# Performance work log

Hardware: AMD Instinct MI355X
Metric: run time of the kernel (lower is better)

The kernel has to match this reference:

```python
import jax, jax.numpy as jnp
import numpy as np

N_REACHES = 4096
N_STEPS = 96
DT = 3600.0  # routing timestep (s), default from MuskingumCungeRouter


def safe_pow(base, exp, eps=1e-6):
    # AD-safe power: exp(e * log(max(b, eps)))
    return jnp.exp(exp * jnp.log(jnp.maximum(base, eps)))


def setup_inputs() -> dict:
    key = jax.random.key(0)
    ks = jax.random.split(key, 10)
    n, T = N_REACHES, N_STEPS
    u = lambda k, lo, hi, shape: jax.random.uniform(k, shape, minval=lo, maxval=hi)
    lateral_inflows = u(ks[0], 0.0, 5.0, (T, n))          # m^3/s lateral inflow
    initial_Q = u(ks[1], 0.1, 10.0, (n,))
    lengths = u(ks[2], 500.0, 10000.0, (n,))              # reach length (m)
    slopes = u(ks[3], 1e-4, 0.05, (n,))                   # bed slope
    manning_n = u(ks[4], 0.02, 0.08, (n,))
    width_coef = u(ks[5], 2.0, 10.0, (n,))
    width_exp = u(ks[6], 0.4, 0.6, (n,))                  # ~0.5 typical
    depth_coef = u(ks[7], 0.2, 0.6, (n,))
    depth_exp = u(ks[8], 0.25, 0.35, (n,))                # ~0.3 typical
    # Strictly lower-triangular sparse adjacency: reach i receives from j < i
    # (valid topological order), ~4 upstream links per reach on average.
    upstream_mask = jnp.tril(jax.random.uniform(ks[9], (n, n)) < (4.0 / n), k=-1)
    is_outlet = jnp.arange(n) == n - 1
    return dict(lateral_inflows=lateral_inflows, initial_Q=initial_Q,
                lengths=lengths, slopes=slopes, manning_n=manning_n,
                width_coef=width_coef, width_exp=width_exp,
                depth_coef=depth_coef, depth_exp=depth_exp,
                upstream_mask=upstream_mask, is_outlet=is_outlet)


def _mc_coeffs(Q, L, S, mn, wc, we, dc, de, dt):
    """Vectorized Muskingum-Cunge coefficients for all reaches.

    Faithful fusion of compute_channel_geometry -> compute_velocity_manning ->
    compute_celerity -> compute_muskingum_params. Q here is Q_ref = max(state.Q, 0.1),
    which only depends on the previous state, so hoisting out of the per-reach
    scan is mathematically identical to the original.
    """
    Qs = jnp.maximum(Q, 0.01)
    W = wc * safe_pow(Qs, we)
    D = dc * safe_pow(Qs, de)
    A = W * D
    R = A / (W + 2.0 * D)                      # hydraulic radius
    safe_S = jnp.maximum(S, 1e-6)
    V = (1.0 / jnp.maximum(mn, 1e-3)) * safe_pow(R, 2.0 / 3.0) * jnp.sqrt(safe_S)
    c = jnp.maximum((5.0 / 3.0) * V, 0.01)     # kinematic wave celerity
    K = jnp.maximum(L / c, dt * 0.1)
    X = jnp.clip(0.5 * (1.0 - Q / (W * c * safe_S * L + 1e-6)), 0.0, 0.5)
    den = 2.0 * K * (1.0 - X) + dt
    C0 = jnp.maximum((dt - 2.0 * K * X) / den, 0.0)
    C1 = jnp.maximum((dt + 2.0 * K * X) / den, 0.0)
    C2 = jnp.maximum((2.0 * K * (1.0 - X) - dt) / den, 0.0)
    tot = C0 + C1 + C2
    return C0 / tot, C1 / tot, C2 / tot


def _route(lateral_inflows, initial_Q, lengths, slopes, manning_n,
           width_coef, width_exp, depth_coef, depth_exp,
           upstream_mask, is_outlet, dt=DT):
    n = lengths.shape[0]

    def step(state, lateral):
        Q, Q_prev, I_prev = state
        Q_ref = jnp.maximum(Q, 0.1)
        C0, C1, C2 = _mc_coeffs(Q_ref, lengths, slopes, manning_n,
                                width_coef, width_exp, depth_coef, depth_exp, dt)

        # Sequential topological sweep: masked reduction over already-routed reaches.
        def process(Q_acc, i):
            upstream_Q = jnp.sum(jnp.where(upstream_mask[i], Q_acc, 0.0))
            I_curr = upstream_Q + lateral[i]
            Q_out = jnp.maximum(C0[i] * I_curr + C1[i] * I_prev[i] + C2[i] * Q_prev[i], 0.0)
            return Q_acc.at[i].set(Q_out), I_curr

        Q_final, I_all = jax.lax.scan(process, jnp.zeros(n, lateral.dtype), jnp.arange(n))
        outlet_Q = jnp.sum(jnp.where(is_outlet, Q_final, 0.0))
        return (Q_final, Q, I_all), outlet_Q

    init = (initial_Q, initial_Q, jnp.zeros(n, initial_Q.dtype))
    _, outlet_series = jax.lax.scan(step, init, lateral_inflows)
    return outlet_series  # [n_timesteps]


def reference(lateral_inflows, initial_Q, lengths, slopes, manning_n,
              width_coef, width_exp, depth_coef, depth_exp,
              upstream_mask, is_outlet):
    return _route(lateral_inflows, initial_Q, lengths, slopes, manning_n,
                  width_coef, width_exp, depth_coef, depth_exp,
                  upstream_mask, is_outlet)
```

## Files before the change

### kernel.cpp

```cpp
#include <hip/hip_runtime.h>

#define NR 4096
#define NT 96
#define NNZ_CAP 10240
#define SREM_CAP 4096
#define LONG_CAP 4096
#define WLDS 8
#define SSTR 4112
#define SHORTLAG 7
#define DHIST 32
#define DTSTEP 3600.0f
#define LOG2_1E6 -19.931568f

__device__ __forceinline__ float RCP(float x) { return __builtin_amdgcn_rcpf(x); }
__device__ __forceinline__ float EXP2(float x) { return __builtin_amdgcn_exp2f(x); }
__device__ __forceinline__ float LOG2(float x) { return __builtin_amdgcn_logf(x); }

__device__ __forceinline__ void phase_barrier() {
  asm volatile("s_waitcnt lgkmcnt(0) vmcnt(12)" ::: "memory");
  __builtin_amdgcn_s_barrier();
  asm volatile("" ::: "memory");
}

__global__ void mc_build(const int* __restrict__ mask, int* __restrict__ rowBase,
                         int* __restrict__ rowCnt, int* __restrict__ gctr,
                         unsigned short* __restrict__ cols) {
  __shared__ unsigned short tmp[80];
  __shared__ int baseS;
  int row = blockIdx.x;
  int lane = threadIdx.x;
  const int* rs = mask + (size_t)row * NR;
  int total = 0;
  for (int j0 = 0; j0 < NR; j0 += 64) {
    int j = j0 + lane;
    int pred = (rs[j] != 0);
    unsigned long long m = __ballot(pred);
    if (pred) {
      int pos = total + __popcll(m & ((1ull << lane) - 1ull));
      if (pos < 80) tmp[pos] = (unsigned short)j;
    }
    total += __popcll(m);
  }
  if (total > 80) total = 80;
  if (lane == 0) {
    int b = atomicAdd(gctr, total);
    rowBase[row] = b;
    rowCnt[row] = total;
    baseS = b;
  }
  __syncthreads();
  int base = baseS;
  for (int e = lane; e < total; e += 64) {
    int p = base + e;
    if (p < NNZ_CAP) cols[p] = tmp[e];
  }
}

__global__ __launch_bounds__(1024) void mc_prep(
    const int* __restrict__ rowBase, const int* __restrict__ rowCnt,
    const int* __restrict__ gctr, const unsigned short* __restrict__ colsOld,
    unsigned short* __restrict__ orderG, unsigned short* __restrict__ levNG,
    unsigned short* __restrict__ scolG, unsigned int* __restrict__ sremMeta,
    unsigned int* __restrict__ longMeta, unsigned short* __restrict__ sremG,
    unsigned short* __restrict__ longG, unsigned char* __restrict__ lsG,
    int* __restrict__ meta) {
  __shared__ unsigned short cols_s[NNZ_CAP];
  __shared__ unsigned char lev_s[NR];
  __shared__ unsigned short newid_s[NR];
  __shared__ unsigned short order_s[NR];
  __shared__ unsigned char lsrc_s[NR];
  __shared__ int cnt[1024];
  __shared__ int ws16[16];
  __shared__ int flagA[40];
  __shared__ int maxLevS;
  const int tid = threadIdx.x;
  int nnz = gctr[0];
  if (nnz > NNZ_CAP) nnz = NNZ_CAP;
  for (int e = tid; e < nnz; e += 1024) cols_s[e] = colsOld[e];
  for (int i = tid; i < 40; i += 1024) flagA[i] = 0;

  int b_r[4], e_r[4];
#pragma unroll
  for (int k = 0; k < 4; ++k) {
    int i = 4 * tid + k;
    int b = rowBase[i];
    if (b > NNZ_CAP) b = NNZ_CAP;
    int e = b + rowCnt[i];
    if (e > NNZ_CAP) e = NNZ_CAP;
    b_r[k] = b;
    e_r[k] = e;
    lev_s[i] = 0;
    lsrc_s[i] = 0;
  }
  if (tid == 0) maxLevS = 0;
  __syncthreads();

  for (int pass = 0; pass < 34; ++pass) {
    int ch = 0;
#pragma unroll
    for (int k = 0; k < 4; ++k) {
      int i = 4 * tid + k;
      int lv = 0;
      for (int e = b_r[k]; e < e_r[k]; ++e) {
        int l2 = (int)lev_s[cols_s[e]] + 1;
        lv = lv > l2 ? lv : l2;
      }
      if (lv > 60) lv = 60;
      if (lv > (int)lev_s[i]) {
        lev_s[i] = (unsigned char)lv;
        ch = 1;
      }
    }
    if (ch) flagA[pass] = 1;
    __syncthreads();
    if (flagA[pass] == 0) break;
  }
  int lm = 0;
#pragma unroll
  for (int k = 0; k < 4; ++k) {
    int l = lev_s[4 * tid + k];
    lm = lm > l ? lm : l;
  }
  atomicMax(&maxLevS, lm);
  __syncthreads();
  const int maxLev = maxLevS;
  if (tid == 0) {
    meta[0] = maxLev + 1;
    meta[2] = (maxLev >= 32) ? 1 : 0;
  }
  if (maxLev >= 32) {
#pragma unroll
    for (int k = 0; k < 4; ++k) {
      int i = 4 * tid + k;
      orderG[i] = (unsigned short)i;
      levNG[i] = (unsigned short)lev_s[i];
    }
    return;
  }

  cnt[tid] = 0;
  __syncthreads();
  int bkt_r[4];
#pragma unroll
  for (int k = 0; k < 4; ++k) {
    int i = 4 * tid + k;
    int d = e_r[k] - b_r[k];
    if (d > 31) d = 31;
    int bkt = ((int)lev_s[i]) * 32 + d;
    bkt_r[k] = bkt;
    atomicAdd(&cnt[bkt], 1);
  }
  __syncthreads();
  {
    int v = cnt[tid];
    int lane = tid & 63, wid = tid >> 6;
    int x = v;
#pragma unroll
    for (int off = 1; off < 64; off <<= 1) {
      int y = __shfl_up(x, off);
      if (lane >= off) x += y;
    }
    if (lane == 63) ws16[wid] = x;
    __syncthreads();
    if (wid == 0) {
      int wv = (lane < 16) ? ws16[lane] : 0;
#pragma unroll
      for (int off = 1; off < 16; off <<= 1) {
        int y = __shfl_up(wv, off);
        if (lane >= off) wv += y;
      }
      if (lane < 16) ws16[lane] = wv;
    }
    __syncthreads();
    int base = wid ? ws16[wid - 1] : 0;
    cnt[tid] = base + x - v;
  }
  __syncthreads();
#pragma unroll
  for (int k = 0; k < 4; ++k) {
    int i = 4 * tid + k;
    int pos = atomicAdd(&cnt[bkt_r[k]], 1);
    order_s[pos] = (unsigned short)i;
    newid_s[i] = (unsigned short)pos;
  }
  __syncthreads();

#pragma unroll
  for (int k = 0; k < 4; ++k) {
    int p = 4 * tid + k;
    int oldi = order_s[p];
    orderG[p] = (unsigned short)oldi;
    int lp = (int)lev_s[oldi];
    levNG[p] = (unsigned short)lp;
    int b = rowBase[oldi];
    if (b > NNZ_CAP) b = NNZ_CAP;
    int e = b + rowCnt[oldi];
    if (e > NNZ_CAP) e = NNZ_CAP;
    int nS = 0, nR = 0, nL = 0;
    for (int ee = b; ee < e; ++ee) {
      int lag = lp - (int)lev_s[cols_s[ee]];
      if (lag <= SHORTLAG) {
        if (nS < 4) ++nS; else ++nR;
      } else ++nL;
    }
    if (nR > 63) nR = 63;
    if (nL > 63) nL = 63;
    int sB = nR ? atomicAdd(&meta[4], nR) : 0;
    int lB = nL ? atomicAdd(&meta[5], nL) : 0;
    if (sB > SREM_CAP) sB = SREM_CAP;
    if (sB + nR > SREM_CAP) nR = SREM_CAP - sB;
    if (lB > LONG_CAP) lB = LONG_CAP;
    if (lB + nL > LONG_CAP) nL = LONG_CAP - lB;
    unsigned short sc[4] = {16384, 16384, 16384, 16384};
    int iS = 0, cR = 0, cL = 0;
    for (int ee = b; ee < e; ++ee) {
      int cOld = cols_s[ee];
      int cN = newid_s[cOld];
      int lag = lp - (int)lev_s[cOld];
      if (lag <= SHORTLAG) {
        if (iS < 4) sc[iS++] = (unsigned short)(cN << 2);
        else if (cR < nR) { sremG[sB + cR] = (unsigned short)(cN << 2); ++cR; }
      } else {
        if (cL < nL) { longG[lB + cL] = (unsigned short)(cN << 2); ++cL; }
        lsrc_s[cN] = 1;
      }
    }
    scolG[4 * p + 0] = sc[0];
    scolG[4 * p + 1] = sc[1];
    scolG[4 * p + 2] = sc[2];
    scolG[4 * p + 3] = sc[3];
    sremMeta[p] = (unsigned)sB | ((unsigned)nR << 20);
    longMeta[p] = (unsigned)lB | ((unsigned)nL << 20);
  }
  if (tid == 0) meta[1] = newid_s[NR - 1];
  __syncthreads();
#pragma unroll
  for (int k = 0; k < 4; ++k) {
    int p = 4 * tid + k;
    lsG[p] = lsrc_s[p];
  }
}

__global__ void mc_permlat(const float* __restrict__ lat,
                           const unsigned short* __restrict__ orderG,
                           float* __restrict__ latP) {
  int g = blockIdx.x * 256 + threadIdx.x;
  int t = g >> 12, p = g & 4095;
  latP[g] = lat[t * NR + orderG[p]];
}

__global__ __launch_bounds__(1024, 4) void mc_route(
    const float* __restrict__ lat, const float* __restrict__ latP,
    const float* __restrict__ initQ, const float* __restrict__ Lg,
    const float* __restrict__ Sg, const float* __restrict__ mng,
    const float* __restrict__ wcg, const float* __restrict__ weg,
    const float* __restrict__ dcg, const float* __restrict__ deg,
    const int* __restrict__ rowBase, const int* __restrict__ rowCnt,
    const unsigned short* __restrict__ colsOld,
    const unsigned short* __restrict__ orderG,
    const unsigned short* __restrict__ levNG,
    const unsigned short* __restrict__ scolG,
    const unsigned int* __restrict__ sremMeta,
    const unsigned int* __restrict__ longMeta,
    const unsigned short* __restrict__ sremG,
    const unsigned short* __restrict__ longG,
    const unsigned char* __restrict__ lsG, const int* __restrict__ meta,
    float* Qhist, float* __restrict__ out, int usePerm) {
  __shared__ float win_s[WLDS * SSTR];
  __shared__ unsigned short srem_s[SREM_CAP];
  __shared__ unsigned short long_s[LONG_CAP];
  const int tid = threadIdx.x;
  const int nlv = meta[0];
  const int fb = meta[2];
  const int outletNew = meta[1];
  const float* latB = usePerm ? latP : lat;

  if (!fb) {
    int sc_r[4][4];
    int lev_r[4], io_r[4], ls_r[4], wOff_r[4];
    unsigned int smeta_r[4], lmeta_r[4];
    const float* latcol_r[4];
    float lwc_r[4], we_r[4], ldc_r[4], de_r[4], lvk_r[4], lgSL_r[4], L_r[4];
    float ip_r[4], q1_r[4], q2_r[4], latN_r[4];

    int nSrem = meta[4];
    if (nSrem > SREM_CAP) nSrem = SREM_CAP;
    int nLong = meta[5];
    if (nLong > LONG_CAP) nLong = LONG_CAP;
    for (int e = tid; e < nSrem; e += 1024) srem_s[e] = sremG[e];
    for (int e = tid; e < nLong; e += 1024) long_s[e] = longG[e];
    if (tid < WLDS) win_s[tid * SSTR + 4096] = 0.f;

#pragma unroll
    for (int k = 0; k < 4; ++k) {
      int p = tid + k * 1024;
      int oldi = orderG[p];
      lev_r[k] = (int)levNG[p];
      uint2 cc = *(const uint2*)(scolG + 4 * p);
      sc_r[k][0] = cc.x & 0xFFFFu;
      sc_r[k][1] = cc.x >> 16;
      sc_r[k][2] = cc.y & 0xFFFFu;
      sc_r[k][3] = cc.y >> 16;
      smeta_r[k] = sremMeta[p];
      lmeta_r[k] = longMeta[p];
      ls_r[k] = (int)lsG[p];
      io_r[k] = (p == outletNew);
      float Lv = Lg[oldi];
      float sS = fmaxf(Sg[oldi], 1e-6f);
      float mnv = fmaxf(mng[oldi], 1e-3f);
      lvk_r[k] = 0.7369656f + 0.5f * LOG2(sS) - LOG2(mnv);
      lgSL_r[k] = LOG2(sS * Lv);
      L_r[k] = Lv;
      lwc_r[k] = LOG2(wcg[oldi]);
      we_r[k] = weg[oldi];
      ldc_r[k] = LOG2(dcg[oldi]);
      de_r[k] = deg[oldi];
      float q0 = initQ[oldi];
      q1_r[k] = q0;
      q2_r[k] = q0;
      ip_r[k] = 0.f;
      wOff_r[k] = 0;
      latcol_r[k] = latB + (usePerm ? p : oldi);
      latN_r[k] = *latcol_r[k];
    }
    __syncthreads();

#define BODY(k, tt)                                                             \
  {                                                                             \
    const int p = tid + (k)*1024;                                               \
    const float latv = latN_r[k];                                               \
    int tn = (tt) + 1;                                                          \
    tn = tn < NT ? tn : NT - 1;                                                 \
    latN_r[k] = latcol_r[k][tn << 12];                                          \
    const char* wb = (const char*)win_s + wOff_r[k];                            \
    float v0 = *(const float*)(wb + sc_r[k][0]);                                \
    float v1 = *(const float*)(wb + sc_r[k][1]);                                \
    float v2 = *(const float*)(wb + sc_r[k][2]);                                \
    float v3 = *(const float*)(wb + sc_r[k][3]);                                \
    float ssum = 0.f;                                                           \
    const int sC = (int)((smeta_r[k] >> 20) & 63);                              \
    if (sC) {                                                                   \
      const int sB = (int)(smeta_r[k] & 0xFFFFFu);                              \
      for (int e = 0; e < sC; ++e)                                              \
        ssum += *(const float*)(wb + srem_s[sB + e]);                           \
    }                                                                           \
    float lsum = 0.f;                                                           \
    const int lC = (int)(lmeta_r[k] >> 20);                                     \
    if (lC) {                                                                   \
      const int lB = (int)(lmeta_r[k] & 0xFFFFFu);                              \
      const char* qb = (const char*)Qhist + (((tt) & 31) << 14);                \
      for (int e = 0; e < lC; ++e) lsum += *(const float*)(qb + long_s[lB + e]);\
    }                                                                           \
    float Qref = fmaxf(q1_r[k], 0.1f);                                          \
    float lq = LOG2(Qref);                                                      \
    float lgW = fmaf(we_r[k], lq, lwc_r[k]);                                    \
    float W = EXP2(lgW);                                                        \
    float aD = fmaf(de_r[k], lq, ldc_r[k]);                                     \
    float Dd = EXP2(aD);                                                        \
    float lgR = fmaxf(lgW + aD - LOG2(fmaf(2.f, Dd, W)), LOG2_1E6);             \
    float lgc = fmaf(0.66666667f, lgR, lvk_r[k]);                               \
    float K = fmaxf(L_r[k] * EXP2(-lgc), 360.f);                                \
    float ratio = EXP2(lq - lgW - lgc - lgSL_r[k]);                             \
    float X = fmaxf(fmaf(-0.5f, ratio, 0.5f), 0.f);                             \
    float twoK = K + K;                                                         \
    float twoKX = twoK * X;                                                     \
    float C0 = fmaxf(DTSTEP - twoKX, 0.f);                                      \
    float C1 = DTSTEP + twoKX;                                                  \
    float C2 = fmaxf(twoK - twoKX - DTSTEP, 0.f);                               \
    float inv = RCP(C0 + C1 + C2);                                              \
    float sup = ((v0 + v1) + (v2 + v3)) + (ssum + lsum);                        \
    float Icurr = sup + latv;                                                   \
    float Qout = fmaxf((C0 * Icurr + C1 * ip_r[k] + C2 * q2_r[k]) * inv, 0.f);  \
    *(float*)((char*)win_s + wOff_r[k] + (p << 2)) = Qout;                      \
    if (ls_r[k]) Qhist[(((tt) & 31) << 12) | p] = Qout;                         \
    if (io_r[k]) out[tt] = Qout;                                                \
    ip_r[k] = Icurr;                                                            \
    q2_r[k] = q1_r[k];                                                          \
    q1_r[k] = Qout;                                                             \
    wOff_r[k] =                                                                 \
        (wOff_r[k] == (WLDS - 1) * SSTR * 4) ? 0 : wOff_r[k] + SSTR * 4;        \
  }

    for (int s = 0; s < nlv - 1; ++s) {
#pragma unroll
      for (int k = 0; k < 4; ++k) {
        int t = s - lev_r[k];
        if ((unsigned)t < (unsigned)NT) BODY(k, t);
      }
      phase_barrier();
    }
    for (int s = nlv - 1; s < NT; ++s) {
#pragma unroll
      for (int k = 0; k < 4; ++k) {
        int t = s - lev_r[k];
        BODY(k, t);
      }
      phase_barrier();
    }
    for (int s = NT; s < NT + nlv - 1; ++s) {
#pragma unroll
      for (int k = 0; k < 4; ++k) {
        int t = s - lev_r[k];
        if ((unsigned)t < (unsigned)NT) BODY(k, t);
      }
      phase_barrier();
    }
  } else {
    unsigned short* colsF = (unsigned short*)win_s;
    int b_r[4], e_r[4], lev_r[4];
    float lwc_r[4], we_r[4], ldc_r[4], de_r[4], lvk_r[4], SL_r[4], L_r[4];
    float ip_r[4], q1_r[4], q2_r[4];
    for (int e = tid; e < NNZ_CAP; e += 1024) colsF[e] = colsOld[e];
#pragma unroll
    for (int k = 0; k < 4; ++k) {
      int i = tid + k * 1024;
      lev_r[k] = (int)levNG[i];
      int b = rowBase[i];
      if (b > NNZ_CAP) b = NNZ_CAP;
      int e = b + rowCnt[i];
      if (e > NNZ_CAP) e = NNZ_CAP;
      b_r[k] = b;
      e_r[k] = e;
      float Lv = Lg[i];
      float sS = fmaxf(Sg[i], 1e-6f);
      float mnv = fmaxf(mng[i], 1e-3f);
      lvk_r[k] = 0.7369656f + 0.5f * LOG2(sS) - LOG2(mnv);
      SL_r[k] = sS * Lv;
      L_r[k] = Lv;
      lwc_r[k] = LOG2(wcg[i]);
      we_r[k] = weg[i];
      ldc_r[k] = LOG2(dcg[i]);
      de_r[k] = deg[i];
      float q0 = initQ[i];
      q1_r[k] = q0;
      q2_r[k] = q0;
      ip_r[k] = 0.f;
    }
    __syncthreads();
    for (int t = 0; t < NT; ++t) {
      for (int l = 0; l < nlv; ++l) {
#pragma unroll
        for (int k = 0; k < 4; ++k) {
          if (lev_r[k] == l) {
            int i = tid + k * 1024;
            float latv = lat[t * NR + i];
            float Qref = fmaxf(q1_r[k], 0.1f);
            float lq = LOG2(Qref);
            float lgW = fmaf(we_r[k], lq, lwc_r[k]);
            float W = EXP2(lgW);
            float aD = fmaf(de_r[k], lq, ldc_r[k]);
            float Dd = EXP2(aD);
            float lgR = fmaxf(lgW + aD - LOG2(fmaf(2.f, Dd, W)), LOG2_1E6);
            float c = fmaxf(EXP2(fmaf(0.66666667f, lgR, lvk_r[k])), 0.01f);
            float K = fmaxf(L_r[k] * RCP(c), 360.f);
            float X =
                fmaxf(0.5f - 0.5f * Qref * RCP(fmaf(W * c, SL_r[k], 1e-6f)), 0.f);
            float twoKX = 2.f * K * X;
            float C0 = fmaxf(DTSTEP - twoKX, 0.f);
            float C1 = DTSTEP + twoKX;
            float C2 = fmaxf(2.f * K - twoKX - DTSTEP, 0.f);
            float inv = RCP(C0 + C1 + C2);
            float sup = 0.f;
            for (int e = b_r[k]; e < e_r[k]; ++e) sup += Qhist[colsF[e]];
            float Icurr = sup + latv;
            float Qout =
                fmaxf((C0 * Icurr + C1 * ip_r[k] + C2 * q2_r[k]) * inv, 0.f);
            Qhist[i] = Qout;
            ip_r[k] = Icurr;
            q2_r[k] = q1_r[k];
            q1_r[k] = Qout;
            if (i == NR - 1) out[t] = Qout;
          }
        }
        __syncthreads();
      }
    }
  }
}

extern "C" void kernel_launch(void* const* d_in, const int* in_sizes, int n_in,
                              void* d_out, int out_size, void* d_ws, size_t ws_size,
                              hipStream_t stream) {
  const float* lat = (const float*)d_in[0];
  const float* iQ = (const float*)d_in[1];
  const float* Lg = (const float*)d_in[2];
  const float* Sg = (const float*)d_in[3];
  const float* mng = (const float*)d_in[4];
  const float* wcg = (const float*)d_in[5];
  const float* weg = (const float*)d_in[6];
  const float* dcg = (const float*)d_in[7];
  const float* deg = (const float*)d_in[8];
  const int* mask = (const int*)d_in[9];
  float* out = (float*)d_out;

  char* w = (char*)d_ws;
  int* rowBase = (int*)w;                        w += NR * 4;
  int* rowCnt = (int*)w;                         w += NR * 4;
  int* gctr = (int*)w;                           w += 16;
  int* meta = (int*)w;                           w += 32;
  unsigned short* colsOld = (unsigned short*)w;  w += NNZ_CAP * 2;
  unsigned short* orderG = (unsigned short*)w;   w += NR * 2;
  unsigned short* levNG = (unsigned short*)w;    w += NR * 2;
  unsigned short* scolG = (unsigned short*)w;    w += NR * 4 * 2;
  unsigned int* sremMeta = (unsigned int*)w;     w += NR * 4;
  unsigned int* longMeta = (unsigned int*)w;     w += NR * 4;
  unsigned short* sremG = (unsigned short*)w;    w += SREM_CAP * 2;
  unsigned short* longG = (unsigned short*)w;    w += LONG_CAP * 2;
  unsigned char* lsG = (unsigned char*)w;        w += NR;
  w += 16 - ((size_t)w & 15);
  float* Qhist = (float*)w;                      w += (size_t)DHIST * NR * 4;
  float* latP = (float*)w;                       w += (size_t)NT * NR * 4;
  size_t need = (size_t)(w - (char*)d_ws);
  int usePerm = (ws_size >= need) ? 1 : 0;

  hipMemsetAsync(gctr, 0, 48, stream);
  mc_build<<<NR, 64, 0, stream>>>(mask, rowBase, rowCnt, gctr, colsOld);
  mc_prep<<<1, 1024, 0, stream>>>(rowBase, rowCnt, gctr, colsOld, orderG, levNG,
                                  scolG, sremMeta, longMeta, sremG, longG, lsG,
                                  meta);
  if (usePerm)
    mc_permlat<<<(NT * NR) / 256, 256, 0, stream>>>(lat, orderG, latP);
  mc_route<<<1, 1024, 0, stream>>>(lat, latP, iQ, Lg, Sg, mng, wcg, weg, dcg,
                                   deg, rowBase, rowCnt, colsOld, orderG, levNG,
                                   scolG, sremMeta, longMeta, sremG, longG, lsG,
                                   meta, Qhist, out, usePerm);
}
```

Measured before the change: 478.9 us.

## Fuse graph prep and routing into one kernel, dropping lateral permutation pass

Merges the single-block level/ordering prep kernel and the routing kernel into one kernel, aliasing prep scratch into the routing window's LDS and keeping the per-reach metadata tables in shared memory instead of global buffers. It also removes the separate kernel that permuted lateral inflows into level order, so routing reads lat through the original reach index. This saves two kernel launches and a global round trip of the metadata and the permuted lateral array. In exchange, lateral reads inside the route loop become scattered gathers rather than contiguous ones, and LDS aliasing adds some risk.

```diff
diff --git a/kernel.cpp b/kernel.cpp
--- a/kernel.cpp
+++ b/kernel.cpp
@@ -56,30 +56,48 @@
   }
 }
 
-__global__ __launch_bounds__(1024) void mc_prep(
-    const int* __restrict__ rowBase, const int* __restrict__ rowCnt,
-    const int* __restrict__ gctr, const unsigned short* __restrict__ colsOld,
-    unsigned short* __restrict__ orderG, unsigned short* __restrict__ levNG,
-    unsigned short* __restrict__ scolG, unsigned int* __restrict__ sremMeta,
-    unsigned int* __restrict__ longMeta, unsigned short* __restrict__ sremG,
-    unsigned short* __restrict__ longG, unsigned char* __restrict__ lsG,
-    int* __restrict__ meta) {
-  __shared__ unsigned short cols_s[NNZ_CAP];
-  __shared__ unsigned char lev_s[NR];
-  __shared__ unsigned short newid_s[NR];
-  __shared__ unsigned short order_s[NR];
-  __shared__ unsigned char lsrc_s[NR];
-  __shared__ int cnt[1024];
+__global__ __launch_bounds__(1024, 4) void mc_fused(
+    const float* __restrict__ lat, const float* __restrict__ initQ,
+    const float* __restrict__ Lg, const float* __restrict__ Sg,
+    const float* __restrict__ mng, const float* __restrict__ wcg,
+    const float* __restrict__ weg, const float* __restrict__ dcg,
+    const float* __restrict__ deg, const int* __restrict__ rowBase,
+    const int* __restrict__ rowCnt, const int* __restrict__ gctr,
+    const unsigned short* __restrict__ colsOld, float* Qhist,
+    float* __restrict__ out) {
+  __shared__ float win_s[WLDS * SSTR];
+  __shared__ unsigned short srem_s[SREM_CAP];
+  __shared__ unsigned short long_s[LONG_CAP];
   __shared__ int ws16[16];
   __shared__ int flagA[40];
-  __shared__ int maxLevS;
+  __shared__ int maxLevS, sremCur, longCur, outletS;
+
+  char* base = (char*)win_s;
+  unsigned short* cols_s = (unsigned short*)(base);
+  unsigned char* lev_s = (unsigned char*)(base + 20480);
+  unsigned char* lsrc_s = (unsigned char*)(base + 24576);
+  unsigned short* newid_s = (unsigned short*)(base + 28672);
+  unsigned short* order_s = (unsigned short*)(base + 36864);
+  int* cnt = (int*)(base + 45056);
+  unsigned short* scolT = (unsigned short*)(base + 49152);
+  unsigned int* smetaT = (unsigned int*)(base + 81920);
+  unsigned int* lmetaT = (unsigned int*)(base + 98304);
+  unsigned short* levT = (unsigned short*)(base + 114688);
+  unsigned short* oldiT = (unsigned short*)(base + 122880);
+
   const int tid = threadIdx.x;
   int nnz = gctr[0];
   if (nnz > NNZ_CAP) nnz = NNZ_CAP;
   for (int e = tid; e < nnz; e += 1024) cols_s[e] = colsOld[e];
   for (int i = tid; i < 40; i += 1024) flagA[i] = 0;
-
-  int b_r[4], e_r[4];
+  if (tid == 0) {
+    maxLevS = 0;
+    sremCur = 0;
+    longCur = 0;
+    outletS = 0;
+  }
+
+  int pb_r[4], pe_r[4];
 #pragma unroll
   for (int k = 0; k < 4; ++k) {
     int i = 4 * tid + k;
@@ -87,12 +105,11 @@
     if (b > NNZ_CAP) b = NNZ_CAP;
     int e = b + rowCnt[i];
     if (e > NNZ_CAP) e = NNZ_CAP;
-    b_r[k] = b;
-    e_r[k] = e;
+    pb_r[k] = b;
+    pe_r[k] = e;
     lev_s[i] = 0;
     lsrc_s[i] = 0;
   }
-  if (tid == 0) maxLevS = 0;
   __syncthreads();
 
   for (int pass = 0; pass < 34; ++pass) {
@@ -101,7 +118,7 @@
     for (int k = 0; k < 4; ++k) {
       int i = 4 * tid + k;
       int lv = 0;
-      for (int e = b_r[k]; e < e_r[k]; ++e) {
+      for (int e = pb_r[k]; e < pe_r[k]; ++e) {
         int l2 = (int)lev_s[cols_s[e]] + 1;
         lv = lv > l2 ? lv : l2;
       }
@@ -115,25 +132,86 @@
     __syncthreads();
     if (flagA[pass] == 0) break;
   }
-  int lm = 0;
-#pragma unroll
-  for (int k = 0; k < 4; ++k) {
-    int l = lev_s[4 * tid + k];
-    lm = lm > l ? lm : l;
-  }
-  atomicMax(&maxLevS, lm);
+  {
+    int lm = 0;
+#pragma unroll
+    for (int k = 0; k < 4; ++k) {
+      int l = lev_s[4 * tid + k];
+      lm = lm > l ? lm : l;
+    }
+    atomicMax(&maxLevS, lm);
+  }
   __syncthreads();
   const int maxLev = maxLevS;
-  if (tid == 0) {
-    meta[0] = maxLev + 1;
-    meta[2] = (maxLev >= 32) ? 1 : 0;
-  }
+  const int nlv = maxLev + 1;
+
   if (maxLev >= 32) {
-#pragma unroll
-    for (int k = 0; k < 4; ++k) {
-      int i = 4 * tid + k;
-      orderG[i] = (unsigned short)i;
-      levNG[i] = (unsigned short)lev_s[i];
+    int b_r[4], e_r[4], lev_r[4];
+    float lwc_r[4], we_r[4], ldc_r[4], de_r[4], lvk_r[4], SL_r[4], L_r[4];
+    float ip_r[4], q1_r[4], q2_r[4];
+#pragma unroll
+    for (int k = 0; k < 4; ++k) {
+      int i = tid + k * 1024;
+      lev_r[k] = (int)lev_s[i];
+      int b = rowBase[i];
+      if (b > NNZ_CAP) b = NNZ_CAP;
+      int e = b + rowCnt[i];
+      if (e > NNZ_CAP) e = NNZ_CAP;
+      b_r[k] = b;
+      e_r[k] = e;
+      float Lv = Lg[i];
+      float sS = fmaxf(Sg[i], 1e-6f);
+      float mnv = fmaxf(mng[i], 1e-3f);
+      lvk_r[k] = 0.7369656f + 0.5f * LOG2(sS) - LOG2(mnv);
+      SL_r[k] = sS * Lv;
+      L_r[k] = Lv;
+      lwc_r[k] = LOG2(wcg[i]);
+      we_r[k] = weg[i];
+      ldc_r[k] = LOG2(dcg[i]);
+      de_r[k] = deg[i];
+      float q0 = initQ[i];
+      q1_r[k] = q0;
+      q2_r[k] = q0;
+      ip_r[k] = 0.f;
+    }
+    __syncthreads();
+    for (int t = 0; t < NT; ++t) {
+      for (int l = 0; l < nlv; ++l) {
+#pragma unroll
+        for (int k = 0; k < 4; ++k) {
+          if (lev_r[k] == l) {
+            int i = tid + k * 1024;
+            float latv = lat[t * NR + i];
+            float Qref = fmaxf(q1_r[k], 0.1f);
+            float lq = LOG2(Qref);
+            float lgW = fmaf(we_r[k], lq, lwc_r[k]);
+            float W = EXP2(lgW);
+            float aD = fmaf(de_r[k], lq, ldc_r[k]);
+            float Dd = EXP2(aD);
+            float lgR = fmaxf(lgW + aD - LOG2(fmaf(2.f, Dd, W)), LOG2_1E6);
+            float c = fmaxf(EXP2(fmaf(0.66666667f, lgR, lvk_r[k])), 0.01f);
+            float K = fmaxf(L_r[k] * RCP(c), 360.f);
+            float X =
+                fmaxf(0.5f - 0.5f * Qref * RCP(fmaf(W * c, SL_r[k], 1e-6f)), 0.f);
+            float twoKX = 2.f * K * X;
+            float C0 = fmaxf(DTSTEP - twoKX, 0.f);
+            float C1 = DTSTEP + twoKX;
+            float C2 = fmaxf(2.f * K - twoKX - DTSTEP, 0.f);
+            float inv = RCP(C0 + C1 + C2);
+            float sup = 0.f;
+            for (int e = b_r[k]; e < e_r[k]; ++e) sup += Qhist[cols_s[e]];
+            float Icurr = sup + latv;
+            float Qout =
+                fmaxf((C0 * Icurr + C1 * ip_r[k] + C2 * q2_r[k]) * inv, 0.f);
+            Qhist[i] = Qout;
+            ip_r[k] = Icurr;
+            q2_r[k] = q1_r[k];
+            q1_r[k] = Qout;
+            if (i == NR - 1) out[t] = Qout;
+          }
+        }
+        __syncthreads();
+      }
     }
     return;
   }
@@ -144,7 +222,7 @@
 #pragma unroll
   for (int k = 0; k < 4; ++k) {
     int i = 4 * tid + k;
-    int d = e_r[k] - b_r[k];
+    int d = pe_r[k] - pb_r[k];
     if (d > 31) d = 31;
     int bkt = ((int)lev_s[i]) * 32 + d;
     bkt_r[k] = bkt;
@@ -172,8 +250,8 @@
       if (lane < 16) ws16[lane] = wv;
     }
     __syncthreads();
-    int base = wid ? ws16[wid - 1] : 0;
-    cnt[tid] = base + x - v;
+    int sb = wid ? ws16[wid - 1] : 0;
+    cnt[tid] = sb + x - v;
   }
   __syncthreads();
 #pragma unroll
@@ -189,9 +267,7 @@
   for (int k = 0; k < 4; ++k) {
     int p = 4 * tid + k;
     int oldi = order_s[p];
-    orderG[p] = (unsigned short)oldi;
     int lp = (int)lev_s[oldi];
-    levNG[p] = (unsigned short)lp;
     int b = rowBase[oldi];
     if (b > NNZ_CAP) b = NNZ_CAP;
     int e = b + rowCnt[oldi];
@@ -205,8 +281,8 @@
     }
     if (nR > 63) nR = 63;
     if (nL > 63) nL = 63;
-    int sB = nR ? atomicAdd(&meta[4], nR) : 0;
-    int lB = nL ? atomicAdd(&meta[5], nL) : 0;
+    int sB = nR ? atomicAdd(&sremCur, nR) : 0;
+    int lB = nL ? atomicAdd(&longCur, nL) : 0;
     if (sB > SREM_CAP) sB = SREM_CAP;
     if (sB + nR > SREM_CAP) nR = SREM_CAP - sB;
     if (lB > LONG_CAP) lB = LONG_CAP;
@@ -219,111 +295,66 @@
       int lag = lp - (int)lev_s[cOld];
       if (lag <= SHORTLAG) {
         if (iS < 4) sc[iS++] = (unsigned short)(cN << 2);
-        else if (cR < nR) { sremG[sB + cR] = (unsigned short)(cN << 2); ++cR; }
+        else if (cR < nR) { srem_s[sB + cR] = (unsigned short)(cN << 2); ++cR; }
       } else {
-        if (cL < nL) { longG[lB + cL] = (unsigned short)(cN << 2); ++cL; }
+        if (cL < nL) { long_s[lB + cL] = (unsigned short)(cN << 2); ++cL; }
         lsrc_s[cN] = 1;
       }
     }
-    scolG[4 * p + 0] = sc[0];
-    scolG[4 * p + 1] = sc[1];
-    scolG[4 * p + 2] = sc[2];
-    scolG[4 * p + 3] = sc[3];
-    sremMeta[p] = (unsigned)sB | ((unsigned)nR << 20);
-    longMeta[p] = (unsigned)lB | ((unsigned)nL << 20);
-  }
-  if (tid == 0) meta[1] = newid_s[NR - 1];
-  __syncthreads();
+    scolT[4 * p + 0] = sc[0];
+    scolT[4 * p + 1] = sc[1];
+    scolT[4 * p + 2] = sc[2];
+    scolT[4 * p + 3] = sc[3];
+    smetaT[p] = (unsigned)sB | ((unsigned)nR << 20);
+    lmetaT[p] = (unsigned)lB | ((unsigned)nL << 20);
+    levT[p] = (unsigned short)lp;
+    oldiT[p] = (unsigned short)oldi;
+    if (oldi == NR - 1) outletS = p;
+  }
+  __syncthreads();
+
+  int sc_r[4][4];
+  int lev_r[4], io_r[4], ls_r[4], wOff_r[4];
+  unsigned int smeta_r[4], lmeta_r[4];
+  const float* latcol_r[4];
+  float lwc_r[4], we_r[4], ldc_r[4], de_r[4], lvk_r[4], lgSL_r[4], L_r[4];
+  float ip_r[4], q1_r[4], q2_r[4], latN_r[4];
+  const int outletNew = outletS;
 #pragma unroll
   for (int k = 0; k < 4; ++k) {
-    int p = 4 * tid + k;
-    lsG[p] = lsrc_s[p];
-  }
-}
-
-__global__ void mc_permlat(const float* __restrict__ lat,
-                           const unsigned short* __restrict__ orderG,
-                           float* __restrict__ latP) {
-  int g = blockIdx.x * 256 + threadIdx.x;
-  int t = g >> 12, p = g & 4095;
-  latP[g] = lat[t * NR + orderG[p]];
-}
-
-__global__ __launch_bounds__(1024, 4) void mc_route(
-    const float* __restrict__ lat, const float* __restrict__ latP,
-    const float* __restrict__ initQ, const float* __restrict__ Lg,
-    const float* __restrict__ Sg, const float* __restrict__ mng,
-    const float* __restrict__ wcg, const float* __restrict__ weg,
-    const float* __restrict__ dcg, const float* __restrict__ deg,
-    const int* __restrict__ rowBase, const int* __restrict__ rowCnt,
-    const unsigned short* __restrict__ colsOld,
-    const unsigned short* __restrict__ orderG,
-    const unsigned short* __restrict__ levNG,
-    const unsigned short* __restrict__ scolG,
-    const unsigned int* __restrict__ sremMeta,
-    const unsigned int* __restrict__ longMeta,
-    const unsigned short* __restrict__ sremG,
-    const unsigned short* __restrict__ longG,
-    const unsigned char* __restrict__ lsG, const int* __restrict__ meta,
-    float* Qhist, float* __restrict__ out, int usePerm) {
-  __shared__ float win_s[WLDS * SSTR];
-  __shared__ unsigned short srem_s[SREM_CAP];
-  __shared__ unsigned short long_s[LONG_CAP];
-  const int tid = threadIdx.x;
-  const int nlv = meta[0];
-  const int fb = meta[2];
-  const int outletNew = meta[1];
-  const float* latB = usePerm ? latP : lat;
-
-  if (!fb) {
-    int sc_r[4][4];
-    int lev_r[4], io_r[4], ls_r[4], wOff_r[4];
-    unsigned int smeta_r[4], lmeta_r[4];
-    const float* latcol_r[4];
-    float lwc_r[4], we_r[4], ldc_r[4], de_r[4], lvk_r[4], lgSL_r[4], L_r[4];
-    float ip_r[4], q1_r[4], q2_r[4], latN_r[4];
-
-    int nSrem = meta[4];
-    if (nSrem > SREM_CAP) nSrem = SREM_CAP;
-    int nLong = meta[5];
-    if (nLong > LONG_CAP) nLong = LONG_CAP;
-    for (int e = tid; e < nSrem; e += 1024) srem_s[e] = sremG[e];
-    for (int e = tid; e < nLong; e += 1024) long_s[e] = longG[e];
-    if (tid < WLDS) win_s[tid * SSTR + 4096] = 0.f;
-
-#pragma unroll
-    for (int k = 0; k < 4; ++k) {
-      int p = tid + k * 1024;
-      int oldi = orderG[p];
-      lev_r[k] = (int)levNG[p];
-      uint2 cc = *(const uint2*)(scolG + 4 * p);
-      sc_r[k][0] = cc.x & 0xFFFFu;
-      sc_r[k][1] = cc.x >> 16;
-      sc_r[k][2] = cc.y & 0xFFFFu;
-      sc_r[k][3] = cc.y >> 16;
-      smeta_r[k] = sremMeta[p];
-      lmeta_r[k] = longMeta[p];
-      ls_r[k] = (int)lsG[p];
-      io_r[k] = (p == outletNew);
-      float Lv = Lg[oldi];
-      float sS = fmaxf(Sg[oldi], 1e-6f);
-      float mnv = fmaxf(mng[oldi], 1e-3f);
-      lvk_r[k] = 0.7369656f + 0.5f * LOG2(sS) - LOG2(mnv);
-      lgSL_r[k] = LOG2(sS * Lv);
-      L_r[k] = Lv;
-      lwc_r[k] = LOG2(wcg[oldi]);
-      we_r[k] = weg[oldi];
-      ldc_r[k] = LOG2(dcg[oldi]);
-      de_r[k] = deg[oldi];
-      float q0 = initQ[oldi];
-      q1_r[k] = q0;
-      q2_r[k] = q0;
-      ip_r[k] = 0.f;
-      wOff_r[k] = 0;
-      latcol_r[k] = latB + (usePerm ? p : oldi);
-      latN_r[k] = *latcol_r[k];
-    }
-    __syncthreads();
+    int p = tid + k * 1024;
+    int oldi = oldiT[p];
+    lev_r[k] = (int)levT[p];
+    uint2 cc = *(const uint2*)(scolT + 4 * p);
+    sc_r[k][0] = cc.x & 0xFFFFu;
+    sc_r[k][1] = cc.x >> 16;
+    sc_r[k][2] = cc.y & 0xFFFFu;
+    sc_r[k][3] = cc.y >> 16;
+    smeta_r[k] = smetaT[p];
+    lmeta_r[k] = lmetaT[p];
+    ls_r[k] = (int)lsrc_s[p];
+    io_r[k] = (p == outletNew);
+    float Lv = Lg[oldi];
+    float sS = fmaxf(Sg[oldi], 1e-6f);
+    float mnv = fmaxf(mng[oldi], 1e-3f);
+    lvk_r[k] = 0.7369656f + 0.5f * LOG2(sS) - LOG2(mnv);
+    lgSL_r[k] = LOG2(sS * Lv);
+    L_r[k] = Lv;
+    lwc_r[k] = LOG2(wcg[oldi]);
+    we_r[k] = weg[oldi];
+    ldc_r[k] = LOG2(dcg[oldi]);
+    de_r[k] = deg[oldi];
+    float q0 = initQ[oldi];
+    q1_r[k] = q0;
+    q2_r[k] = q0;
+    ip_r[k] = 0.f;
+    wOff_r[k] = 0;
+    latcol_r[k] = lat + oldi;
+    latN_r[k] = *latcol_r[k];
+  }
+  __syncthreads();
+  if (tid < WLDS) win_s[tid * SSTR + 4096] = 0.f;
+  __syncthreads();
 
 #define BODY(k, tt)                                                             \
   {                                                                             \
@@ -381,100 +412,29 @@
         (wOff_r[k] == (WLDS - 1) * SSTR * 4) ? 0 : wOff_r[k] + SSTR * 4;        \
   }
 
-    for (int s = 0; s < nlv - 1; ++s) {
-#pragma unroll
-      for (int k = 0; k < 4; ++k) {
-        int t = s - lev_r[k];
-        if ((unsigned)t < (unsigned)NT) BODY(k, t);
-      }
-      phase_barrier();
-    }
-    for (int s = nlv - 1; s < NT; ++s) {
-#pragma unroll
-      for (int k = 0; k < 4; ++k) {
-        int t = s - lev_r[k];
-        BODY(k, t);
-      }
-      phase_barrier();
-    }
-    for (int s = NT; s < NT + nlv - 1; ++s) {
-#pragma unroll
-      for (int k = 0; k < 4; ++k) {
-        int t = s - lev_r[k];
-        if ((unsigned)t < (unsigned)NT) BODY(k, t);
-      }
-      phase_barrier();
-    }
-  } else {
-    unsigned short* colsF = (unsigned short*)win_s;
-    int b_r[4], e_r[4], lev_r[4];
-    float lwc_r[4], we_r[4], ldc_r[4], de_r[4], lvk_r[4], SL_r[4], L_r[4];
-    float ip_r[4], q1_r[4], q2_r[4];
-    for (int e = tid; e < NNZ_CAP; e += 1024) colsF[e] = colsOld[e];
-#pragma unroll
-    for (int k = 0; k < 4; ++k) {
-      int i = tid + k * 1024;
-      lev_r[k] = (int)levNG[i];
-      int b = rowBase[i];
-      if (b > NNZ_CAP) b = NNZ_CAP;
-      int e = b + rowCnt[i];
-      if (e > NNZ_CAP) e = NNZ_CAP;
-      b_r[k] = b;
-      e_r[k] = e;
-      float Lv = Lg[i];
-      float sS = fmaxf(Sg[i], 1e-6f);
-      float mnv = fmaxf(mng[i], 1e-3f);
-      lvk_r[k] = 0.7369656f + 0.5f * LOG2(sS) - LOG2(mnv);
-      SL_r[k] = sS * Lv;
-      L_r[k] = Lv;
-      lwc_r[k] = LOG2(wcg[i]);
-      we_r[k] = weg[i];
-      ldc_r[k] = LOG2(dcg[i]);
-      de_r[k] = deg[i];
-      float q0 = initQ[i];
-      q1_r[k] = q0;
-      q2_r[k] = q0;
-      ip_r[k] = 0.f;
-    }
-    __syncthreads();
-    for (int t = 0; t < NT; ++t) {
-      for (int l = 0; l < nlv; ++l) {
-#pragma unroll
-        for (int k = 0; k < 4; ++k) {
-          if (lev_r[k] == l) {
-            int i = tid + k * 1024;
-            float latv = lat[t * NR + i];
-            float Qref = fmaxf(q1_r[k], 0.1f);
-            float lq = LOG2(Qref);
-            float lgW = fmaf(we_r[k], lq, lwc_r[k]);
-            float W = EXP2(lgW);
-            float aD = fmaf(de_r[k], lq, ldc_r[k]);
-            float Dd = EXP2(aD);
-            float lgR = fmaxf(lgW + aD - LOG2(fmaf(2.f, Dd, W)), LOG2_1E6);
-            float c = fmaxf(EXP2(fmaf(0.66666667f, lgR, lvk_r[k])), 0.01f);
-            float K = fmaxf(L_r[k] * RCP(c), 360.f);
-            float X =
-                fmaxf(0.5f - 0.5f * Qref * RCP(fmaf(W * c, SL_r[k], 1e-6f)), 0.f);
-            float twoKX = 2.f * K * X;
-            float C0 = fmaxf(DTSTEP - twoKX, 0.f);
-            float C1 = DTSTEP + twoKX;
-            float C2 = fmaxf(2.f * K - twoKX - DTSTEP, 0.f);
-            float inv = RCP(C0 + C1 + C2);
-            float sup = 0.f;
-            for (int e = b_r[k]; e < e_r[k]; ++e) sup += Qhist[colsF[e]];
-            float Icurr = sup + latv;
-            float Qout =
-                fmaxf((C0 * Icurr + C1 * ip_r[k] + C2 * q2_r[k]) * inv, 0.f);
-            Qhist[i] = Qout;
-            ip_r[k] = Icurr;
-            q2_r[k] = q1_r[k];
-            q1_r[k] = Qout;
-            if (i == NR - 1) out[t] = Qout;
-          }
-        }
-        __syncthreads();
-      }
-    }
+  for (int s = 0; s < nlv - 1; ++s) {
+#pragma unroll
+    for (int k = 0; k < 4; ++k) {
+      int t = s - lev_r[k];
+      if ((unsigned)t < (unsigned)NT) BODY(k, t);
+    }
+    phase_barrier();
+  }
+  for (int s = nlv - 1; s < NT; ++s) {
+#pragma unroll
+    for (int k = 0; k < 4; ++k) {
+      int t = s - lev_r[k];
+      BODY(k, t);
+    }
+    phase_barrier();
+  }
+  for (int s = NT; s < NT + nlv - 1; ++s) {
+#pragma unroll
+    for (int k = 0; k < 4; ++k) {
+      int t = s - lev_r[k];
+      if ((unsigned)t < (unsigned)NT) BODY(k, t);
+    }
+    phase_barrier();
   }
 }
 
@@ -497,31 +457,12 @@
   int* rowBase = (int*)w;                        w += NR * 4;
   int* rowCnt = (int*)w;                         w += NR * 4;
   int* gctr = (int*)w;                           w += 16;
-  int* meta = (int*)w;                           w += 32;
   unsigned short* colsOld = (unsigned short*)w;  w += NNZ_CAP * 2;
-  unsigned short* orderG = (unsigned short*)w;   w += NR * 2;
-  unsigned short* levNG = (unsigned short*)w;    w += NR * 2;
-  unsigned short* scolG = (unsigned short*)w;    w += NR * 4 * 2;
-  unsigned int* sremMeta = (unsigned int*)w;     w += NR * 4;
-  unsigned int* longMeta = (unsigned int*)w;     w += NR * 4;
-  unsigned short* sremG = (unsigned short*)w;    w += SREM_CAP * 2;
-  unsigned short* longG = (unsigned short*)w;    w += LONG_CAP * 2;
-  unsigned char* lsG = (unsigned char*)w;        w += NR;
   w += 16 - ((size_t)w & 15);
   float* Qhist = (float*)w;                      w += (size_t)DHIST * NR * 4;
-  float* latP = (float*)w;                       w += (size_t)NT * NR * 4;
-  size_t need = (size_t)(w - (char*)d_ws);
-  int usePerm = (ws_size >= need) ? 1 : 0;
-
-  hipMemsetAsync(gctr, 0, 48, stream);
+
+  hipMemsetAsync(gctr, 0, 16, stream);
   mc_build<<<NR, 64, 0, stream>>>(mask, rowBase, rowCnt, gctr, colsOld);
-  mc_prep<<<1, 1024, 0, stream>>>(rowBase, rowCnt, gctr, colsOld, orderG, levNG,
-                                  scolG, sremMeta, longMeta, sremG, longG, lsG,
-                                  meta);
-  if (usePerm)
-    mc_permlat<<<(NT * NR) / 256, 256, 0, stream>>>(lat, orderG, latP);
-  mc_route<<<1, 1024, 0, stream>>>(lat, latP, iQ, Lg, Sg, mng, wcg, weg, dcg,
-                                   deg, rowBase, rowCnt, colsOld, orderG, levNG,
-                                   scolG, sremMeta, longMeta, sremG, longG, lsG,
-                                   meta, Qhist, out, usePerm);
+  mc_fused<<<1, 1024, 0, stream>>>(lat, iQ, Lg, Sg, mng, wcg, weg, dcg, deg,
+                                   rowBase, rowCnt, gctr, colsOld, Qhist, out);
 }
```

Result: slower. 496.2 us (+3.6%).

## Split per-reach update into pre and post phases off the critical path

Applied to the files above, without the earlier changes.

Each reach's step is split into a PRE phase and a POST phase. PRE runs one diagonal ahead and gathers upstream contributions with lag ≥2 (short-range and long-range history), then computes the Muskingum coefficients for the next step. POST only sums lag-1 upstream values plus overflow lag-1 entries and applies the update. Upstream lists are repartitioned into pre and post segments, and the spill buffer capacity is doubled. The intent is to shorten the dependent chain between barriers, at the cost of more registers, a merged loop with per-iteration guards, and a larger LDS footprint.

```diff
diff --git a/kernel.cpp b/kernel.cpp
--- a/kernel.cpp
+++ b/kernel.cpp
@@ -3,7 +3,7 @@
 #define NR 4096
 #define NT 96
 #define NNZ_CAP 10240
-#define SREM_CAP 4096
+#define SREM_CAP 8192
 #define LONG_CAP 4096
 #define WLDS 8
 #define SSTR 4112
@@ -196,40 +196,55 @@
     if (b > NNZ_CAP) b = NNZ_CAP;
     int e = b + rowCnt[oldi];
     if (e > NNZ_CAP) e = NNZ_CAP;
-    int nS = 0, nR = 0, nL = 0;
+    int nL1 = 0, nPre = 0, nL = 0;
     for (int ee = b; ee < e; ++ee) {
       int lag = lp - (int)lev_s[cols_s[ee]];
-      if (lag <= SHORTLAG) {
-        if (nS < 4) ++nS; else ++nR;
-      } else ++nL;
-    }
-    if (nR > 63) nR = 63;
+      if (lag > SHORTLAG) ++nL;
+      else if (lag == 1) ++nL1;
+      else ++nPre;
+    }
+    int nPost = nL1 > 4 ? nL1 - 4 : 0;
+    if (nPre > 63) nPre = 63;
+    if (nPost > 63) nPost = 63;
     if (nL > 63) nL = 63;
-    int sB = nR ? atomicAdd(&meta[4], nR) : 0;
+    int sLen = nPre + nPost;
+    int sB = sLen ? atomicAdd(&meta[4], sLen) : 0;
     int lB = nL ? atomicAdd(&meta[5], nL) : 0;
     if (sB > SREM_CAP) sB = SREM_CAP;
-    if (sB + nR > SREM_CAP) nR = SREM_CAP - sB;
+    if (sB + sLen > SREM_CAP) {
+      sLen = SREM_CAP - sB;
+      if (nPre > sLen) nPre = sLen;
+      nPost = sLen - nPre;
+    }
     if (lB > LONG_CAP) lB = LONG_CAP;
     if (lB + nL > LONG_CAP) nL = LONG_CAP - lB;
     unsigned short sc[4] = {16384, 16384, 16384, 16384};
-    int iS = 0, cR = 0, cL = 0;
+    int iS = 0, cPre = 0, cPost = 0, cL = 0;
     for (int ee = b; ee < e; ++ee) {
       int cOld = cols_s[ee];
       int cN = newid_s[cOld];
       int lag = lp - (int)lev_s[cOld];
-      if (lag <= SHORTLAG) {
-        if (iS < 4) sc[iS++] = (unsigned short)(cN << 2);
-        else if (cR < nR) { sremG[sB + cR] = (unsigned short)(cN << 2); ++cR; }
-      } else {
+      if (lag > SHORTLAG) {
         if (cL < nL) { longG[lB + cL] = (unsigned short)(cN << 2); ++cL; }
         lsrc_s[cN] = 1;
+      } else if (lag == 1) {
+        if (iS < 4) sc[iS++] = (unsigned short)(cN << 2);
+        else if (cPost < nPost) {
+          sremG[sB + nPre + cPost] = (unsigned short)(cN << 2);
+          ++cPost;
+        }
+      } else {
+        if (cPre < nPre) {
+          sremG[sB + cPre] = (unsigned short)(cN << 2);
+          ++cPre;
+        }
       }
     }
     scolG[4 * p + 0] = sc[0];
     scolG[4 * p + 1] = sc[1];
     scolG[4 * p + 2] = sc[2];
     scolG[4 * p + 3] = sc[3];
-    sremMeta[p] = (unsigned)sB | ((unsigned)nR << 20);
+    sremMeta[p] = (unsigned)sB | ((unsigned)nPre << 20) | ((unsigned)nPost << 26);
     longMeta[p] = (unsigned)lB | ((unsigned)nL << 20);
   }
   if (tid == 0) meta[1] = newid_s[NR - 1];
@@ -282,6 +297,7 @@
     const float* latcol_r[4];
     float lwc_r[4], we_r[4], ldc_r[4], de_r[4], lvk_r[4], lgSL_r[4], L_r[4];
     float ip_r[4], q1_r[4], q2_r[4], latN_r[4];
+    float psum_r[4], C0_r[4], C1_r[4], C2_r[4], inv_r[4];
 
     int nSrem = meta[4];
     if (nSrem > SREM_CAP) nSrem = SREM_CAP;
@@ -319,38 +335,79 @@
       q1_r[k] = q0;
       q2_r[k] = q0;
       ip_r[k] = 0.f;
+      psum_r[k] = 0.f;
       wOff_r[k] = 0;
       latcol_r[k] = latB + (usePerm ? p : oldi);
       latN_r[k] = *latcol_r[k];
+      float Qref = fmaxf(q0, 0.1f);
+      float lq = LOG2(Qref);
+      float lgW = fmaf(we_r[k], lq, lwc_r[k]);
+      float W = EXP2(lgW);
+      float aD = fmaf(de_r[k], lq, ldc_r[k]);
+      float Dd = EXP2(aD);
+      float lgR = fmaxf(lgW + aD - LOG2(fmaf(2.f, Dd, W)), LOG2_1E6);
+      float lgc = fmaf(0.66666667f, lgR, lvk_r[k]);
+      float K = fmaxf(Lv * EXP2(-lgc), 360.f);
+      float ratio = EXP2(lq - lgW - lgc - lgSL_r[k]);
+      float X = fmaxf(fmaf(-0.5f, ratio, 0.5f), 0.f);
+      float twoK = K + K;
+      float twoKX = twoK * X;
+      C0_r[k] = fmaxf(DTSTEP - twoKX, 0.f);
+      C1_r[k] = DTSTEP + twoKX;
+      C2_r[k] = fmaxf(twoK - twoKX - DTSTEP, 0.f);
+      inv_r[k] = RCP(C0_r[k] + C1_r[k] + C2_r[k]);
     }
     __syncthreads();
 
-#define BODY(k, tt)                                                             \
+#define POST(k, tt)                                                             \
   {                                                                             \
     const int p = tid + (k)*1024;                                               \
-    const float latv = latN_r[k];                                               \
-    int tn = (tt) + 1;                                                          \
-    tn = tn < NT ? tn : NT - 1;                                                 \
-    latN_r[k] = latcol_r[k][tn << 12];                                          \
     const char* wb = (const char*)win_s + wOff_r[k];                            \
     float v0 = *(const float*)(wb + sc_r[k][0]);                                \
     float v1 = *(const float*)(wb + sc_r[k][1]);                                \
     float v2 = *(const float*)(wb + sc_r[k][2]);                                \
     float v3 = *(const float*)(wb + sc_r[k][3]);                                \
-    float ssum = 0.f;                                                           \
-    const int sC = (int)((smeta_r[k] >> 20) & 63);                              \
-    if (sC) {                                                                   \
+    float ext = 0.f;                                                            \
+    const int nPost = (int)(smeta_r[k] >> 26);                                  \
+    if (nPost) {                                                                \
+      const int sBp = (int)(smeta_r[k] & 0xFFFFFu) +                            \
+                      (int)((smeta_r[k] >> 20) & 63);                           \
+      for (int e = 0; e < nPost; ++e)                                           \
+        ext += *(const float*)(wb + srem_s[sBp + e]);                           \
+    }                                                                           \
+    float sup = psum_r[k] + ((v0 + v1) + (v2 + v3)) + ext;                      \
+    float Icurr = sup + latN_r[k];                                              \
+    float Qout = fmaxf(                                                         \
+        (C0_r[k] * Icurr + C1_r[k] * ip_r[k] + C2_r[k] * q2_r[k]) * inv_r[k],   \
+        0.f);                                                                   \
+    *(float*)((char*)win_s + wOff_r[k] + (p << 2)) = Qout;                      \
+    if (ls_r[k]) Qhist[(((tt) & 31) << 12) | p] = Qout;                         \
+    if (io_r[k]) out[tt] = Qout;                                                \
+    ip_r[k] = Icurr;                                                            \
+    q2_r[k] = q1_r[k];                                                          \
+    q1_r[k] = Qout;                                                             \
+    wOff_r[k] =                                                                 \
+        (wOff_r[k] == (WLDS - 1) * SSTR * 4) ? 0 : wOff_r[k] + SSTR * 4;        \
+  }
+
+#define PRE(k, tn)                                                              \
+  {                                                                             \
+    latN_r[k] = latcol_r[k][(tn) << 12];                                        \
+    const char* wbn = (const char*)win_s + wOff_r[k];                           \
+    float ps = 0.f;                                                             \
+    const int nPre = (int)((smeta_r[k] >> 20) & 63);                            \
+    if (nPre) {                                                                 \
       const int sB = (int)(smeta_r[k] & 0xFFFFFu);                              \
-      for (int e = 0; e < sC; ++e)                                              \
-        ssum += *(const float*)(wb + srem_s[sB + e]);                           \
+      for (int e = 0; e < nPre; ++e)                                            \
+        ps += *(const float*)(wbn + srem_s[sB + e]);                            \
     }                                                                           \
-    float lsum = 0.f;                                                           \
     const int lC = (int)(lmeta_r[k] >> 20);                                     \
     if (lC) {                                                                   \
       const int lB = (int)(lmeta_r[k] & 0xFFFFFu);                              \
-      const char* qb = (const char*)Qhist + (((tt) & 31) << 14);                \
-      for (int e = 0; e < lC; ++e) lsum += *(const float*)(qb + long_s[lB + e]);\
+      const char* qb = (const char*)Qhist + (((tn) & 31) << 14);                \
+      for (int e = 0; e < lC; ++e) ps += *(const float*)(qb + long_s[lB + e]);  \
     }                                                                           \
+    psum_r[k] = ps;                                                             \
     float Qref = fmaxf(q1_r[k], 0.1f);                                          \
     float lq = LOG2(Qref);                                                      \
     float lgW = fmaf(we_r[k], lq, lwc_r[k]);                                    \
@@ -364,44 +421,23 @@
     float X = fmaxf(fmaf(-0.5f, ratio, 0.5f), 0.f);                             \
     float twoK = K + K;                                                         \
     float twoKX = twoK * X;                                                     \
-    float C0 = fmaxf(DTSTEP - twoKX, 0.f);                                      \
-    float C1 = DTSTEP + twoKX;                                                  \
-    float C2 = fmaxf(twoK - twoKX - DTSTEP, 0.f);                               \
-    float inv = RCP(C0 + C1 + C2);                                              \
-    float sup = ((v0 + v1) + (v2 + v3)) + (ssum + lsum);                        \
-    float Icurr = sup + latv;                                                   \
-    float Qout = fmaxf((C0 * Icurr + C1 * ip_r[k] + C2 * q2_r[k]) * inv, 0.f);  \
-    *(float*)((char*)win_s + wOff_r[k] + (p << 2)) = Qout;                      \
-    if (ls_r[k]) Qhist[(((tt) & 31) << 12) | p] = Qout;                         \
-    if (io_r[k]) out[tt] = Qout;                                                \
-    ip_r[k] = Icurr;                                                            \
-    q2_r[k] = q1_r[k];                                                          \
-    q1_r[k] = Qout;                                                             \
-    wOff_r[k] =                                                                 \
-        (wOff_r[k] == (WLDS - 1) * SSTR * 4) ? 0 : wOff_r[k] + SSTR * 4;        \
-  }
-
-    for (int s = 0; s < nlv - 1; ++s) {
+    C0_r[k] = fmaxf(DTSTEP - twoKX, 0.f);                                       \
+    C1_r[k] = DTSTEP + twoKX;                                                   \
+    C2_r[k] = fmaxf(twoK - twoKX - DTSTEP, 0.f);                                \
+    inv_r[k] = RCP(C0_r[k] + C1_r[k] + C2_r[k]);                                \
+  }
+
+    const int nDiag = NT + nlv - 1;
+    for (int s = 0; s < nDiag; ++s) {
 #pragma unroll
       for (int k = 0; k < 4; ++k) {
         int t = s - lev_r[k];
-        if ((unsigned)t < (unsigned)NT) BODY(k, t);
-      }
-      phase_barrier();
-    }
-    for (int s = nlv - 1; s < NT; ++s) {
+        if ((unsigned)t < (unsigned)NT) POST(k, t);
+      }
 #pragma unroll
       for (int k = 0; k < 4; ++k) {
-        int t = s - lev_r[k];
-        BODY(k, t);
-      }
-      phase_barrier();
-    }
-    for (int s = NT; s < NT + nlv - 1; ++s) {
-#pragma unroll
-      for (int k = 0; k < 4; ++k) {
-        int t = s - lev_r[k];
-        if ((unsigned)t < (unsigned)NT) BODY(k, t);
+        int tn = s + 1 - lev_r[k];
+        if ((unsigned)tn < (unsigned)NT) PRE(k, tn);
       }
       phase_barrier();
     }
```

Measured after the change: 584.0 us. 22.0% more time.
